# Optimization experiments

Hardware: AMD Instinct MI355X
Metric: run time of the kernel (lower is better)

Reference implementation:

```python
import jax, jax.numpy as jnp
import numpy as np

T, N1, N2 = 20, 65536, 4096
BETA = 0.9            # Ensemble leak (beta)
FREQ_BETA = 0.95      # RunningAverage beta
TARGET_FREQ = 0.1
REFRACTORY_GAIN = -0.3
BASE_THRESHOLD = 1.0


def setup_inputs() -> dict:
    key = jax.random.key(0)
    k1, k2 = jax.random.split(key)
    # sensory input per step: signal*0.95+0.05 plus noise -> just uniform here
    x_seq = jax.random.uniform(k1, (T, N1), dtype=jnp.float32)
    # Connection weights: uniform, column-normalized (weights / weights.sum(dim=0))
    W = jax.random.uniform(k2, (N1, N2), dtype=jnp.float32)
    W = W / W.sum(axis=0, keepdims=True)
    return {"x_seq": x_seq, "W": W}


def ensemble_step(state, x):
    # state = (activation, input_gain, threshold, frequency), all [N]
    act, gain, thr, freq = state
    gain = gain + (1.0 - gain) * 0.2                      # gain relaxation toward 1
    act = BETA * act + x * gain + 0.05                    # leaky integration + bias
    spikes = act > thr                                    # bool [N]
    sf = spikes.astype(act.dtype)
    freq = FREQ_BETA * freq + (1.0 - FREQ_BETA) * sf      # running spike frequency
    # homeostatic threshold: raise if too frequent, decay if too rare
    thr = jnp.where(freq > TARGET_FREQ, thr + 0.05,
                    jnp.where(freq < TARGET_FREQ, thr / 1.05, thr))
    gain = jnp.where(spikes, REFRACTORY_GAIN, gain)       # refractory gain
    act = jnp.where(spikes, 0.0, act)                     # 'zero' reset mechanism
    return (act, gain, thr, freq), sf


def reference(x_seq, W):
    n1 = x_seq.shape[1]
    n2 = W.shape[1]

    def init_state(n):
        return (jnp.zeros((n,), jnp.float32),               # activation
                jnp.ones((n,), jnp.float32),                # input_gain
                jnp.full((n,), BASE_THRESHOLD, jnp.float32),# threshold
                jnp.zeros((n,), jnp.float32))               # frequency

    def step(carry, x):
        s1, s2 = carry
        s1, sp1 = ensemble_step(s1, x)       # l1 spikes as float [N1]
        y = sp1 @ W                          # Connection: spike gather-sum matvec -> [N2]
        s2, sp2 = ensemble_step(s2, y)
        # record l2 post-reset activation (continuous, useful baseline signal)
        return (s1, s2), s2[0]

    (_, _), l2_act_hist = jax.lax.scan(step, (init_state(n1), init_state(n2)), x_seq)
    return l2_act_hist  # [T, N2]
```

## Files before the change

kernel.cpp:

```cpp
#include <hip/hip_runtime.h>

#define T 20
#define N1 65536
#define N2 4096

#define ROWS_PER_BLOCK 512
#define COLS_PER_BLOCK 1024

__global__ __launch_bounds__(256) void layer1_kernel(const float* __restrict__ x_seq,
                                                     float* __restrict__ S) {
    int i = blockIdx.x * blockDim.x + threadIdx.x;
    float act = 0.0f, gain = 1.0f, thr = 1.0f, freq = 0.0f;
    float sf_arr[T];
#pragma unroll
    for (int t = 0; t < T; ++t) {
        float x = x_seq[t * N1 + i];
        gain = __fadd_rn(gain, __fmul_rn(__fsub_rn(1.0f, gain), 0.2f));
        act = __fadd_rn(__fadd_rn(__fmul_rn(0.9f, act), __fmul_rn(x, gain)), 0.05f);
        bool sp = act > thr;
        float sf = sp ? 1.0f : 0.0f;
        freq = __fadd_rn(__fmul_rn(0.95f, freq), __fmul_rn(0.05f, sf));
        if (freq > 0.1f)       thr = __fadd_rn(thr, 0.05f);
        else if (freq < 0.1f)  thr = __fdiv_rn(thr, 1.05f);
        gain = sp ? -0.3f : gain;
        act  = sp ? 0.0f  : act;
        sf_arr[t] = sf;
    }
#pragma unroll
    for (int t = 0; t < T; ++t) S[i * T + t] = sf_arr[t];
}

__global__ __launch_bounds__(256) void spike_gemm_kernel(const float* __restrict__ W,
                                                         const float* __restrict__ S,
                                                         float* __restrict__ Y) {
    int cb = blockIdx.x & 3;
    int rb = blockIdx.x >> 2;
    int j  = cb * COLS_PER_BLOCK + threadIdx.x * 4;
    int i0 = rb * ROWS_PER_BLOCK;

    float4 acc[T];
#pragma unroll
    for (int t = 0; t < T; ++t) acc[t] = make_float4(0.f, 0.f, 0.f, 0.f);

    const float4* Wp = reinterpret_cast<const float4*>(W + (size_t)i0 * N2 + j);
    const float*  Sp = S + (size_t)i0 * T;

#pragma unroll 4
    for (int r = 0; r < ROWS_PER_BLOCK; ++r) {
        float4 w = Wp[(size_t)r * (N2 / 4)];
        const float* s = Sp + r * T;
#pragma unroll
        for (int t = 0; t < T; ++t) {
            float sv = s[t];
            acc[t].x += w.x * sv;
            acc[t].y += w.y * sv;
            acc[t].z += w.z * sv;
            acc[t].w += w.w * sv;
        }
    }

#pragma unroll
    for (int t = 0; t < T; ++t) {
        float* y = Y + t * N2 + j;
        atomicAdd(y + 0, acc[t].x);
        atomicAdd(y + 1, acc[t].y);
        atomicAdd(y + 2, acc[t].z);
        atomicAdd(y + 3, acc[t].w);
    }
}

__global__ __launch_bounds__(256) void layer2_kernel(const float* __restrict__ Y,
                                                     float* __restrict__ out) {
    int j = blockIdx.x * blockDim.x + threadIdx.x;
    float act = 0.0f, gain = 1.0f, thr = 1.0f, freq = 0.0f;
#pragma unroll
    for (int t = 0; t < T; ++t) {
        float y = Y[t * N2 + j];
        gain = __fadd_rn(gain, __fmul_rn(__fsub_rn(1.0f, gain), 0.2f));
        act = __fadd_rn(__fadd_rn(__fmul_rn(0.9f, act), __fmul_rn(y, gain)), 0.05f);
        bool sp = act > thr;
        float sf = sp ? 1.0f : 0.0f;
        freq = __fadd_rn(__fmul_rn(0.95f, freq), __fmul_rn(0.05f, sf));
        if (freq > 0.1f)       thr = __fadd_rn(thr, 0.05f);
        else if (freq < 0.1f)  thr = __fdiv_rn(thr, 1.05f);
        gain = sp ? -0.3f : gain;
        act  = sp ? 0.0f  : act;
        out[t * N2 + j] = act;
    }
}

extern "C" void kernel_launch(void* const* d_in, const int* in_sizes, int n_in,
                              void* d_out, int out_size, void* d_ws, size_t ws_size,
                              hipStream_t stream) {
    const float* x_seq = (const float*)d_in[0];
    const float* W     = (const float*)d_in[1];
    float* out = (float*)d_out;

    float* S = (float*)d_ws;
    float* Y = (float*)((char*)d_ws + (size_t)N1 * T * sizeof(float));

    hipMemsetAsync(Y, 0, (size_t)T * N2 * sizeof(float), stream);

    layer1_kernel<<<N1 / 256, 256, 0, stream>>>(x_seq, S);

    int gemm_blocks = (N1 / ROWS_PER_BLOCK) * (N2 / COLS_PER_BLOCK);
    spike_gemm_kernel<<<gemm_blocks, 256, 0, stream>>>(W, S, Y);

    layer2_kernel<<<N2 / 256, 256, 0, stream>>>(Y, out);
}
```

Before: 1.495 ms.

## Bit-pack spikes, skip inactive rows, and replace atomics with partial-sum reduction

Layer-1 spikes are now packed into one 32-bit mask per neuron instead of T floats, which cuts spike traffic and lets the GEMM skip multiply work and silent rows via branches. Float atomics into Y are replaced by per-chunk partial-sum writes, followed by a separate reduce kernel over 256 chunks. The branches are data-dependent and may diverge within a wavefront, although bits are uniform across a block, so they should not diverge. The partial buffer is large (256*20*4096 floats, about 84 MB) and adds write and read traffic plus an extra launch.

```diff
diff --git a/kernel.cpp b/kernel.cpp
--- a/kernel.cpp
+++ b/kernel.cpp
@@ -1,17 +1,19 @@
 #include <hip/hip_runtime.h>
+#include <stdint.h>
 
 #define T 20
 #define N1 65536
 #define N2 4096
 
-#define ROWS_PER_BLOCK 512
-#define COLS_PER_BLOCK 1024
+#define RPB 256
+#define NCHUNK (N1 / RPB)
+#define CPB 1024
 
 __global__ __launch_bounds__(256) void layer1_kernel(const float* __restrict__ x_seq,
-                                                     float* __restrict__ S) {
+                                                     uint32_t* __restrict__ Sbits) {
     int i = blockIdx.x * blockDim.x + threadIdx.x;
     float act = 0.0f, gain = 1.0f, thr = 1.0f, freq = 0.0f;
-    float sf_arr[T];
+    uint32_t bits = 0;
 #pragma unroll
     for (int t = 0; t < T; ++t) {
         float x = x_seq[t * N1 + i];
@@ -24,49 +26,65 @@
         else if (freq < 0.1f)  thr = __fdiv_rn(thr, 1.05f);
         gain = sp ? -0.3f : gain;
         act  = sp ? 0.0f  : act;
-        sf_arr[t] = sf;
+        if (sp) bits |= (1u << t);
     }
+    Sbits[i] = bits;
+}
+
+__device__ __forceinline__ void accum_row(float4* acc, uint32_t bits, const float4& w) {
+    if (bits) {
 #pragma unroll
-    for (int t = 0; t < T; ++t) S[i * T + t] = sf_arr[t];
+        for (int t = 0; t < T; ++t) {
+            if (bits & (1u << t)) {
+                acc[t].x += w.x; acc[t].y += w.y; acc[t].z += w.z; acc[t].w += w.w;
+            }
+        }
+    }
 }
 
 __global__ __launch_bounds__(256) void spike_gemm_kernel(const float* __restrict__ W,
-                                                         const float* __restrict__ S,
-                                                         float* __restrict__ Y) {
+                                                         const uint32_t* __restrict__ Sb,
+                                                         float* __restrict__ P) {
     int cb = blockIdx.x & 3;
     int rb = blockIdx.x >> 2;
-    int j  = cb * COLS_PER_BLOCK + threadIdx.x * 4;
-    int i0 = rb * ROWS_PER_BLOCK;
+    int j  = cb * CPB + threadIdx.x * 4;
+    int i0 = rb * RPB;
 
     float4 acc[T];
 #pragma unroll
     for (int t = 0; t < T; ++t) acc[t] = make_float4(0.f, 0.f, 0.f, 0.f);
 
     const float4* Wp = reinterpret_cast<const float4*>(W + (size_t)i0 * N2 + j);
-    const float*  Sp = S + (size_t)i0 * T;
 
-#pragma unroll 4
-    for (int r = 0; r < ROWS_PER_BLOCK; ++r) {
-        float4 w = Wp[(size_t)r * (N2 / 4)];
-        const float* s = Sp + r * T;
-#pragma unroll
-        for (int t = 0; t < T; ++t) {
-            float sv = s[t];
-            acc[t].x += w.x * sv;
-            acc[t].y += w.y * sv;
-            acc[t].z += w.z * sv;
-            acc[t].w += w.w * sv;
-        }
+    for (int r = 0; r < RPB; r += 4) {
+        uint32_t b0 = Sb[i0 + r + 0];
+        uint32_t b1 = Sb[i0 + r + 1];
+        uint32_t b2 = Sb[i0 + r + 2];
+        uint32_t b3 = Sb[i0 + r + 3];
+        float4 w0 = Wp[(size_t)(r + 0) * (N2 / 4)];
+        float4 w1 = Wp[(size_t)(r + 1) * (N2 / 4)];
+        float4 w2 = Wp[(size_t)(r + 2) * (N2 / 4)];
+        float4 w3 = Wp[(size_t)(r + 3) * (N2 / 4)];
+        accum_row(acc, b0, w0);
+        accum_row(acc, b1, w1);
+        accum_row(acc, b2, w2);
+        accum_row(acc, b3, w3);
     }
 
+    float* Pp = P + (size_t)rb * T * N2;
 #pragma unroll
     for (int t = 0; t < T; ++t) {
-        float* y = Y + t * N2 + j;
-        atomicAdd(y + 0, acc[t].x);
-        atomicAdd(y + 1, acc[t].y);
-        atomicAdd(y + 2, acc[t].z);
-        atomicAdd(y + 3, acc[t].w);
+        *reinterpret_cast<float4*>(Pp + (size_t)t * N2 + j) = acc[t];
     }
+}
+
+__global__ __launch_bounds__(256) void reduce_kernel(const float* __restrict__ P,
+                                                     float* __restrict__ Y) {
+    int idx = blockIdx.x * blockDim.x + threadIdx.x;
+    float s = 0.0f;
+#pragma unroll 8
+    for (int c = 0; c < NCHUNK; ++c) s += P[(size_t)c * T * N2 + idx];
+    Y[idx] = s;
 }
 
 __global__ __launch_bounds__(256) void layer2_kernel(const float* __restrict__ Y,
@@ -96,15 +114,16 @@
     const float* W     = (const float*)d_in[1];
     float* out = (float*)d_out;
 
-    float* S = (float*)d_ws;
-    float* Y = (float*)((char*)d_ws + (size_t)N1 * T * sizeof(float));
+    uint32_t* Sbits = (uint32_t*)d_ws;
+    float* P = (float*)((char*)d_ws + (size_t)N1 * sizeof(uint32_t));
+    float* Y = P + (size_t)NCHUNK * T * N2;
 
-    hipMemsetAsync(Y, 0, (size_t)T * N2 * sizeof(float), stream);
+    layer1_kernel<<<N1 / 256, 256, 0, stream>>>(x_seq, Sbits);
 
-    layer1_kernel<<<N1 / 256, 256, 0, stream>>>(x_seq, S);
+    int gemm_blocks = NCHUNK * (N2 / CPB);
+    spike_gemm_kernel<<<gemm_blocks, 256, 0, stream>>>(W, Sbits, P);
 
-    int gemm_blocks = (N1 / ROWS_PER_BLOCK) * (N2 / COLS_PER_BLOCK);
-    spike_gemm_kernel<<<gemm_blocks, 256, 0, stream>>>(W, S, Y);
+    reduce_kernel<<<(T * N2) / 256, 256, 0, stream>>>(P, Y);
 
     layer2_kernel<<<N2 / 256, 256, 0, stream>>>(Y, out);
 }
```

Result: faster. 1.437 ms (-3.9%).
